# Kernel tuning notes

Hardware: AMD Instinct MI355X
Metric: run time of the kernel (lower is better)

The kernel has to match this reference:

```python
import jax, jax.numpy as jnp
import numpy as np

B, S, HID = 2, 2048, 2048
H, HKV, DH = 32, 8, 64
GROUPS = H // HKV
SCALE = DH ** -0.5
ROPE_THETA = 10000.0
NEG_INF = jnp.finfo(jnp.float32).min


def setup_inputs() -> dict:
    key = jax.random.key(0)
    ks = jax.random.split(key, 6)
    hidden_states = jax.random.normal(ks[0], (B, S, HID), dtype=jnp.float32)
    # true rotary embeddings (HF Llama style): inv_freq over half dim, duplicated
    inv_freq = 1.0 / (ROPE_THETA ** (np.arange(0, DH, 2, dtype=np.float32) / DH))
    freqs = np.arange(S, dtype=np.float32)[:, None] * inv_freq[None, :]  # [S, DH/2]
    emb = np.concatenate([freqs, freqs], axis=-1)                        # [S, DH]
    cos = jnp.broadcast_to(jnp.asarray(np.cos(emb), jnp.float32), (B, S, DH))
    sin = jnp.broadcast_to(jnp.asarray(np.sin(emb), jnp.float32), (B, S, DH))
    # additive causal mask [1,1,S,S]
    causal = jnp.tril(jnp.ones((S, S), dtype=bool))
    attention_mask = jnp.where(causal, 0.0, NEG_INF)[None, None].astype(jnp.float32)
    std = 0.02
    Wq = jax.random.normal(ks[1], (H * DH, HID), dtype=jnp.float32) * std
    Wk = jax.random.normal(ks[2], (HKV * DH, HID), dtype=jnp.float32) * std
    Wv = jax.random.normal(ks[3], (HKV * DH, HID), dtype=jnp.float32) * std
    Wo = jax.random.normal(ks[4], (HID, H * DH), dtype=jnp.float32) * std
    return {"hidden_states": hidden_states, "cos": cos, "sin": sin,
            "attention_mask": attention_mask, "Wq": Wq, "Wk": Wk, "Wv": Wv, "Wo": Wo}


def _rotate_half(x):
    x1, x2 = jnp.split(x, 2, axis=-1)
    return jnp.concatenate([-x2, x1], axis=-1)


def reference(hidden_states, cos, sin, attention_mask, Wq, Wk, Wv, Wo):
    b, s, _ = hidden_states.shape
    # projections -> [B, H(kv), S, DH]
    q = (hidden_states @ Wq.T).reshape(b, s, H, DH).transpose(0, 2, 1, 3)
    k = (hidden_states @ Wk.T).reshape(b, s, HKV, DH).transpose(0, 2, 1, 3)
    v = (hidden_states @ Wv.T).reshape(b, s, HKV, DH).transpose(0, 2, 1, 3)
    # RoPE (cos/sin: [B,S,DH] -> broadcast over head axis)
    c = cos[:, None, :, :]
    sn = sin[:, None, :, :]
    q = q * c + _rotate_half(q) * sn
    k = k * c + _rotate_half(k) * sn
    # GQA: repeat kv heads
    k = jnp.repeat(k, GROUPS, axis=1)  # [B,H,S,DH]
    v = jnp.repeat(v, GROUPS, axis=1)
    # eager attention: full [B,H,S,S] scores in memory
    scores = jnp.einsum('bhqd,bhkd->bhqk', q, k) * SCALE + attention_mask[:, :, :, :s]
    attn = jax.nn.softmax(scores, axis=-1)
    out = jnp.einsum('bhqk,bhkd->bhqd', attn, v)
    out = out.transpose(0, 2, 1, 3).reshape(b, s, H * DH)
    return out @ Wo.T
```

## Files before the change

### kernel.cpp

```cpp
#include <hip/hip_runtime.h>
#include <hip/hip_bf16.h>
#include <cstdint>
#include <cstddef>

#define B_    2
#define S_    2048
#define HID_  2048
#define H_    32
#define HKV_  8
#define DH_   64
#define SC2_  0.1803368801111244f

typedef __bf16 bf16;
typedef bf16  bf16x2 __attribute__((ext_vector_type(2)));
typedef bf16  bf16x4 __attribute__((ext_vector_type(4)));
typedef bf16  bf16x8 __attribute__((ext_vector_type(8)));
typedef float f32x4  __attribute__((ext_vector_type(4)));
typedef float f32x16 __attribute__((ext_vector_type(16)));
typedef uint32_t u32x2 __attribute__((ext_vector_type(2)));

typedef __attribute__((address_space(3))) uint32_t  lds_u32_t;
typedef __attribute__((address_space(1))) const uint32_t glob_u32_t;

__device__ __forceinline__ void async16(const void* g, void* l) {
    __builtin_amdgcn_global_load_lds((glob_u32_t*)g, (lds_u32_t*)l, 16, 0, 0);
}

__device__ __forceinline__ bf16x8 cvt8(float4 a, float4 b) {
    bf16x8 r;
    r[0] = (bf16)a.x; r[1] = (bf16)a.y; r[2] = (bf16)a.z; r[3] = (bf16)a.w;
    r[4] = (bf16)b.x; r[5] = (bf16)b.y; r[6] = (bf16)b.z; r[7] = (bf16)b.w;
    return r;
}

__device__ __forceinline__ uint32_t pkbf(float a, float b) {
    bf16x2 t; t[0] = (bf16)a; t[1] = (bf16)b;
    return __builtin_bit_cast(uint32_t, t);
}
__device__ __forceinline__ bf16x8 mk8(uint32_t a, uint32_t b, uint32_t c, uint32_t d) {
    union { uint32_t u[4]; bf16x8 v; } t;
    t.u[0] = a; t.u[1] = b; t.u[2] = c; t.u[3] = d;
    return t.v;
}

__global__ __launch_bounds__(256) void cvt_all_kernel(
    const float* __restrict__ X,  const float* __restrict__ Wq,
    const float* __restrict__ Wk, const float* __restrict__ Wv,
    const float* __restrict__ Wo,
    bf16* __restrict__ Xb,  bf16* __restrict__ Wqb, bf16* __restrict__ Wkb,
    bf16* __restrict__ Wvb, bf16* __restrict__ Wob)
{
    const int i = blockIdx.x * 256 + threadIdx.x;
    const float* src; bf16* dst; int off;
    if (i < 1048576)      { src = X;  dst = Xb;  off = i; }
    else if (i < 1572864) { src = Wq; dst = Wqb; off = i - 1048576; }
    else if (i < 1703936) { src = Wk; dst = Wkb; off = i - 1572864; }
    else if (i < 1835008) { src = Wv; dst = Wvb; off = i - 1703936; }
    else                  { src = Wo; dst = Wob; off = i - 1835008; }
    float4 a = ((const float4*)src)[2 * off];
    float4 b = ((const float4*)src)[2 * off + 1];
    ((bf16x8*)dst)[off] = cvt8(a, b);
}

__global__ __launch_bounds__(256) void gemm_qkv_kernel(
    const bf16* __restrict__ A,
    const bf16* __restrict__ Wqb, const bf16* __restrict__ Wkb,
    const bf16* __restrict__ Wvb,
    const float* __restrict__ cs, const float* __restrict__ sn,
    bf16* __restrict__ Qo, bf16* __restrict__ Ko, bf16* __restrict__ Vt)
{
    __shared__ bf16 a_lds[128 * 64];
    __shared__ bf16 b_lds[128 * 64];

    const int tid  = threadIdx.x;
    const int wave = tid >> 6;
    const int lane = tid & 63;
    const int quad = lane >> 4;
    const int l16  = lane & 15;
    const int wm   = wave >> 1;
    const int wn   = wave & 1;
    const int m0   = blockIdx.x * 128;
    const int n0   = blockIdx.y * 128;

    f32x4 acc[4][4];
    #pragma unroll
    for (int mt = 0; mt < 4; ++mt)
        #pragma unroll
        for (int nt = 0; nt < 4; ++nt)
            acc[mt][nt] = (f32x4){0.f, 0.f, 0.f, 0.f};

    int srow[4], sgcol[4];
    const bf16* browp[4];
    #pragma unroll
    for (int i = 0; i < 4; ++i) {
        const int e = tid * 8 + i * 2048;
        srow[i] = e >> 6;
        const int chunk = (e >> 3) & 7;
        sgcol[i] = (chunk ^ (srow[i] & 7)) << 3;
        const int n = n0 + srow[i];
        browp[i] = (n < 2048) ? (Wqb + (size_t)n * HID_)
                 : (n < 2560) ? (Wkb + (size_t)(n - 2048) * HID_)
                              : (Wvb + (size_t)(n - 2560) * HID_);
    }

    for (int k0 = 0; k0 < HID_; k0 += 64) {
        #pragma unroll
        for (int i = 0; i < 4; ++i) {
            async16(A + (size_t)(m0 + srow[i]) * HID_ + k0 + sgcol[i],
                    &a_lds[tid * 8 + i * 2048]);
            async16(browp[i] + k0 + sgcol[i],
                    &b_lds[tid * 8 + i * 2048]);
        }
        __syncthreads();
        #pragma unroll
        for (int ks = 0; ks < 2; ++ks) {
            bf16x8 af[4], bfr[4];
            #pragma unroll
            for (int mt = 0; mt < 4; ++mt) {
                const int row = wm * 64 + mt * 16 + l16;
                const int c = (ks * 4 + quad) ^ (row & 7);
                af[mt] = *(const bf16x8*)(&a_lds[row * 64 + c * 8]);
            }
            #pragma unroll
            for (int nt = 0; nt < 4; ++nt) {
                const int row = wn * 64 + nt * 16 + l16;
                const int c = (ks * 4 + quad) ^ (row & 7);
                bfr[nt] = *(const bf16x8*)(&b_lds[row * 64 + c * 8]);
            }
            #pragma unroll
            for (int mt = 0; mt < 4; ++mt)
                #pragma unroll
                for (int nt = 0; nt < 4; ++nt)
                    acc[mt][nt] = __builtin_amdgcn_mfma_f32_16x16x32_bf16(
                        af[mt], bfr[nt], acc[mt][nt], 0, 0, 0);
        }
        __syncthreads();
    }

    const int nw = n0 + wn * 64;
    const int d  = l16;
    #pragma unroll
    for (int mt = 0; mt < 4; ++mt) {
        #pragma unroll
        for (int r = 0; r < 4; ++r) {
            const int m  = m0 + wm * 64 + mt * 16 + quad * 4 + r;
            const int bb = m >> 11;
            const int ss = m & (S_ - 1);
            const float v0 = acc[mt][0][r], v1 = acc[mt][1][r];
            const float v2 = acc[mt][2][r], v3 = acc[mt][3][r];
            if (nw < 2048) {
                const int h = nw >> 6;
                bf16* dp = Qo + ((size_t)(bb * H_ + h) * S_ + ss) * DH_;
                const float* cp = cs + ((size_t)bb * S_ + ss) * DH_;
                const float* sp = sn + ((size_t)bb * S_ + ss) * DH_;
                dp[ 0 + d] = (bf16)((v0 * cp[ 0 + d] - v2 * sp[ 0 + d]) * SC2_);
                dp[16 + d] = (bf16)((v1 * cp[16 + d] - v3 * sp[16 + d]) * SC2_);
                dp[32 + d] = (bf16)((v2 * cp[32 + d] + v0 * sp[32 + d]) * SC2_);
                dp[48 + d] = (bf16)((v3 * cp[48 + d] + v1 * sp[48 + d]) * SC2_);
            } else if (nw < 2560) {
                const int h = (nw - 2048) >> 6;
                bf16* dp = Ko + ((size_t)(bb * HKV_ + h) * S_ + ss) * DH_;
                const float* cp = cs + ((size_t)bb * S_ + ss) * DH_;
                const float* sp = sn + ((size_t)bb * S_ + ss) * DH_;
                dp[ 0 + d] = (bf16)(v0 * cp[ 0 + d] - v2 * sp[ 0 + d]);
                dp[16 + d] = (bf16)(v1 * cp[16 + d] - v3 * sp[16 + d]);
                dp[32 + d] = (bf16)(v2 * cp[32 + d] + v0 * sp[32 + d]);
                dp[48 + d] = (bf16)(v3 * cp[48 + d] + v1 * sp[48 + d]);
            } else {
                const int h = (nw - 2560) >> 6;
                bf16* dp = Vt + ((size_t)(bb * HKV_ + h) * DH_) * S_ + ss;
                dp[(size_t)( 0 + d) * S_] = (bf16)v0;
                dp[(size_t)(16 + d) * S_] = (bf16)v1;
                dp[(size_t)(32 + d) * S_] = (bf16)v2;
                dp[(size_t)(48 + d) * S_] = (bf16)v3;
            }
        }
    }
}

__global__ __launch_bounds__(256) void gemm_out_kernel(
    const bf16* __restrict__ A, const bf16* __restrict__ Wb,
    float* __restrict__ Y)
{
    __shared__ bf16 a_lds[128 * 64];
    __shared__ bf16 b_lds[128 * 64];

    const int tid  = threadIdx.x;
    const int wave = tid >> 6;
    const int lane = tid & 63;
    const int quad = lane >> 4;
    const int l16  = lane & 15;
    const int wm   = wave >> 1;
    const int wn   = wave & 1;
    const int m0   = blockIdx.x * 128;
    const int n0   = blockIdx.y * 128;

    f32x4 acc[4][4];
    #pragma unroll
    for (int mt = 0; mt < 4; ++mt)
        #pragma unroll
        for (int nt = 0; nt < 4; ++nt)
            acc[mt][nt] = (f32x4){0.f, 0.f, 0.f, 0.f};

    int srow[4], sgcol[4];
    #pragma unroll
    for (int i = 0; i < 4; ++i) {
        const int e = tid * 8 + i * 2048;
        srow[i] = e >> 6;
        const int chunk = (e >> 3) & 7;
        sgcol[i] = (chunk ^ (srow[i] & 7)) << 3;
    }

    for (int k0 = 0; k0 < HID_; k0 += 64) {
        #pragma unroll
        for (int i = 0; i < 4; ++i) {
            async16(A + (size_t)(m0 + srow[i]) * HID_ + k0 + sgcol[i],
                    &a_lds[tid * 8 + i * 2048]);
            async16(Wb + (size_t)(n0 + srow[i]) * HID_ + k0 + sgcol[i],
                    &b_lds[tid * 8 + i * 2048]);
        }
        __syncthreads();
        #pragma unroll
        for (int ks = 0; ks < 2; ++ks) {
            bf16x8 af[4], bfr[4];
            #pragma unroll
            for (int mt = 0; mt < 4; ++mt) {
                const int row = wm * 64 + mt * 16 + l16;
                const int c = (ks * 4 + quad) ^ (row & 7);
                af[mt] = *(const bf16x8*)(&a_lds[row * 64 + c * 8]);
            }
            #pragma unroll
            for (int nt = 0; nt < 4; ++nt) {
                const int row = wn * 64 + nt * 16 + l16;
                const int c = (ks * 4 + quad) ^ (row & 7);
                bfr[nt] = *(const bf16x8*)(&b_lds[row * 64 + c * 8]);
            }
            #pragma unroll
            for (int mt = 0; mt < 4; ++mt)
                #pragma unroll
                for (int nt = 0; nt < 4; ++nt)
                    acc[mt][nt] = __builtin_amdgcn_mfma_f32_16x16x32_bf16(
                        af[mt], bfr[nt], acc[mt][nt], 0, 0, 0);
        }
        __syncthreads();
    }

    #pragma unroll
    for (int mt = 0; mt < 4; ++mt)
        #pragma unroll
        for (int nt = 0; nt < 4; ++nt)
            #pragma unroll
            for (int r = 0; r < 4; ++r) {
                const int m = m0 + wm * 64 + mt * 16 + quad * 4 + r;
                const int n = n0 + wn * 64 + nt * 16 + l16;
                Y[(size_t)m * HID_ + n] = acc[mt][nt][r];
            }
}

__global__ __launch_bounds__(256) void attn_kernel(
    const bf16* __restrict__ Q, const bf16* __restrict__ K,
    const bf16* __restrict__ Vt, bf16* __restrict__ O)
{
    __shared__ bf16 k_lds[2][64 * 64];
    __shared__ bf16 v_lds[2][64 * 64];

    const int tid  = threadIdx.x;
    const int wave = tid >> 6;
    const int lane = tid & 63;
    const int l32  = lane & 31;
    const int half = lane >> 5;
    const int h  = blockIdx.y;
    const int b  = blockIdx.z;
    const int hkv = h >> 2;

    const bf16* Qg = Q  + (size_t)(b * H_ + h) * S_ * DH_;
    const bf16* Kg = K  + (size_t)(b * HKV_ + hkv) * S_ * DH_;
    const bf16* Vg = Vt + ((size_t)(b * HKV_ + hkv) * DH_) * S_;

    const int srow0  = tid >> 3;
    const int scolsw = ((tid & 7) ^ ((tid >> 3) & 7)) << 3;

    #pragma unroll 1
    for (int ph = 0; ph < 2; ++ph) {
        const int qt  = ph == 0 ? (int)blockIdx.x : (15 - (int)blockIdx.x);
        const int q0  = qt * 128;
        const int qb0 = q0 + wave * 32;
        const int qa  = qb0 + l32;

        bf16x8 qf[4];
        #pragma unroll
        for (int c = 0; c < 4; ++c)
            qf[c] = *(const bf16x8*)(Qg + (size_t)qa * DH_ + c * 16 + half * 8);

        f32x16 o_acc[2];
        #pragma unroll
        for (int dt = 0; dt < 2; ++dt)
            #pragma unroll
            for (int e = 0; e < 16; ++e) o_acc[dt][e] = 0.f;
        float m_i = -1e30f, l_i = 0.f;

        const int nkt = 2 * qt + 2;

        #pragma unroll
        for (int i = 0; i < 2; ++i) {
            const int row = srow0 + i * 32;
            async16(Kg + (size_t)row * DH_ + scolsw, &k_lds[0][tid * 8 + i * 2048]);
            async16(Vg + (size_t)row * S_  + scolsw, &v_lds[0][tid * 8 + i * 2048]);
        }
        __syncthreads();

        for (int kt = 0; kt < nkt; ++kt) {
            if (kt + 1 < nkt) {
                bf16* kb = k_lds[(kt + 1) & 1];
                bf16* vb = v_lds[(kt + 1) & 1];
                #pragma unroll
                for (int i = 0; i < 2; ++i) {
                    const int row = srow0 + i * 32;
                    async16(Kg + (size_t)((kt + 1) * 64 + row) * DH_ + scolsw,
                            kb + tid * 8 + i * 2048);
                    async16(Vg + (size_t)row * S_ + (kt + 1) * 64 + scolsw,
                            vb + tid * 8 + i * 2048);
                }
            }

            if (kt * 64 <= qb0 + 31) {
                const bf16* kb = k_lds[kt & 1];
                const bf16* vb = v_lds[kt & 1];
                const bool act1 = (kt * 64 + 32) <= (qb0 + 31);

                f32x16 s0, s1;
                {
                    bf16x8 kf[4];
                    #pragma unroll
                    for (int c = 0; c < 4; ++c) {
                        const int col = ((2 * c + half) ^ (l32 & 7)) << 3;
                        kf[c] = *(const bf16x8*)(kb + l32 * 64 + col);
                    }
                    f32x16 a;
                    #pragma unroll
                    for (int e = 0; e < 16; ++e) a[e] = 0.f;
                    __builtin_amdgcn_s_setprio(1);
                    #pragma unroll
                    for (int c = 0; c < 4; ++c)
                        a = __builtin_amdgcn_mfma_f32_32x32x16_bf16(kf[c], qf[c], a, 0, 0, 0);
                    __builtin_amdgcn_s_setprio(0);
                    s0 = a;
                }
                if (act1) {
                    bf16x8 kf[4];
                    #pragma unroll
                    for (int c = 0; c < 4; ++c) {
                        const int row = 32 + l32;
                        const int col = ((2 * c + half) ^ (row & 7)) << 3;
                        kf[c] = *(const bf16x8*)(kb + row * 64 + col);
                    }
                    f32x16 a;
                    #pragma unroll
                    for (int e = 0; e < 16; ++e) a[e] = 0.f;
                    __builtin_amdgcn_s_setprio(1);
                    #pragma unroll
                    for (int c = 0; c < 4; ++c)
                        a = __builtin_amdgcn_mfma_f32_32x32x16_bf16(kf[c], qf[c], a, 0, 0, 0);
                    __builtin_amdgcn_s_setprio(0);
                    s1 = a;
                }

                if (!((kt * 64 + 31) <= qb0)) {
                    const int qrel = qa - kt * 64 - 4 * half;
                    #pragma unroll
                    for (int e = 0; e < 16; ++e)
                        if (((e & 3) + 8 * (e >> 2)) > qrel) s0[e] = -1e30f;
                }
                if (act1 && !((kt * 64 + 63) <= qb0)) {
                    const int qrel = qa - kt * 64 - 32 - 4 * half;
                    #pragma unroll
                    for (int e = 0; e < 16; ++e)
                        if (((e & 3) + 8 * (e >> 2)) > qrel) s1[e] = -1e30f;
                }

                float mx = s0[0];
                #pragma unroll
                for (int e = 1; e < 16; ++e) mx = fmaxf(mx, s0[e]);
                if (act1)
                    #pragma unroll
                    for (int e = 0; e < 16; ++e) mx = fmaxf(mx, s1[e]);
                mx = fmaxf(mx, __shfl_xor(mx, 32));

                float al = 1.f;
                if (!__all(mx <= m_i + 8.f)) {
                    const float mn = fmaxf(m_i, mx);
                    al = exp2f(m_i - mn);
                    m_i = mn;
                    #pragma unroll
                    for (int dt = 0; dt < 2; ++dt)
                        #pragma unroll
                        for (int e = 0; e < 16; ++e) o_acc[dt][e] *= al;
                }

                float sm = 0.f;
                #pragma unroll
                for (int e = 0; e < 16; ++e) {
                    const float pp = exp2f(s0[e] - m_i);
                    s0[e] = pp; sm += pp;
                }
                if (act1)
                    #pragma unroll
                    for (int e = 0; e < 16; ++e) {
                        const float pp = exp2f(s1[e] - m_i);
                        s1[e] = pp; sm += pp;
                    }
                sm += __shfl_xor(sm, 32);
                l_i = l_i * al + sm;

                bf16x8 pf[4];
                {
                    uint32_t d0 = pkbf(s0[0],  s0[1]),  d1 = pkbf(s0[2],  s0[3]);
                    uint32_t d2 = pkbf(s0[4],  s0[5]),  d3 = pkbf(s0[6],  s0[7]);
                    uint32_t d4 = pkbf(s0[8],  s0[9]),  d5 = pkbf(s0[10], s0[11]);
                    uint32_t d6 = pkbf(s0[12], s0[13]), d7 = pkbf(s0[14], s0[15]);
                    u32x2 r02 = __builtin_amdgcn_permlane32_swap(d0, d2, false, false);
                    u32x2 r13 = __builtin_amdgcn_permlane32_swap(d1, d3, false, false);
                    u32x2 r46 = __builtin_amdgcn_permlane32_swap(d4, d6, false, false);
                    u32x2 r57 = __builtin_amdgcn_permlane32_swap(d5, d7, false, false);
                    pf[0] = mk8(r02[0], r13[0], r02[1], r13[1]);
                    pf[1] = mk8(r46[0], r57[0], r46[1], r57[1]);
                }
                if (act1) {
                    uint32_t d0 = pkbf(s1[0],  s1[1]),  d1 = pkbf(s1[2],  s1[3]);
                    uint32_t d2 = pkbf(s1[4],  s1[5]),  d3 = pkbf(s1[6],  s1[7]);
                    uint32_t d4 = pkbf(s1[8],  s1[9]),  d5 = pkbf(s1[10], s1[11]);
                    uint32_t d6 = pkbf(s1[12], s1[13]), d7 = pkbf(s1[14], s1[15]);
                    u32x2 r02 = __builtin_amdgcn_permlane32_swap(d0, d2, false, false);
                    u32x2 r13 = __builtin_amdgcn_permlane32_swap(d1, d3, false, false);
                    u32x2 r46 = __builtin_amdgcn_permlane32_swap(d4, d6, false, false);
                    u32x2 r57 = __builtin_amdgcn_permlane32_swap(d5, d7, false, false);
                    pf[2] = mk8(r02[0], r13[0], r02[1], r13[1]);
                    pf[3] = mk8(r46[0], r57[0], r46[1], r57[1]);
                }

                bf16x8 vf[2][4];
                #pragma unroll
                for (int dt = 0; dt < 2; ++dt)
                    #pragma unroll
                    for (int c = 0; c < 4; ++c) {
                        const int row = dt * 32 + l32;
                        const int col = ((2 * c + half) ^ (row & 7)) << 3;
                        vf[dt][c] = *(const bf16x8*)(vb + row * 64 + col);
                    }

                const int nc = act1 ? 4 : 2;
                __builtin_amdgcn_s_setprio(1);
                #pragma unroll
                for (int c = 0; c < 4; ++c) {
                    if (c >= nc) break;
                    #pragma unroll
                    for (int dt = 0; dt < 2; ++dt)
                        o_acc[dt] = __builtin_amdgcn_mfma_f32_32x32x16_bf16(
                            vf[dt][c], pf[c], o_acc[dt], 0, 0, 0);
                }
                __builtin_amdgcn_s_setprio(0);
            }
            __syncthreads();
        }

        const float inv = 1.f / l_i;
        bf16* op = O + ((size_t)(b * S_ + qa) * H_ + h) * DH_;
        #pragma unroll
        for (int dt = 0; dt < 2; ++dt)
            #pragma unroll
            for (int g = 0; g < 4; ++g) {
                bf16x4 ov;
                #pragma unroll
                for (int r = 0; r < 4; ++r) ov[r] = (bf16)(o_acc[dt][g * 4 + r] * inv);
                *(bf16x4*)(op + dt * 32 + g * 8 + half * 4) = ov;
            }
        __syncthreads();
    }
}

extern "C" void kernel_launch(void* const* d_in, const int* in_sizes, int n_in,
                              void* d_out, int out_size, void* d_ws, size_t ws_size,
                              hipStream_t stream)
{
    const float* X    = (const float*)d_in[0];
    const float* cs   = (const float*)d_in[1];
    const float* sn   = (const float*)d_in[2];
    const float* Wq   = (const float*)d_in[4];
    const float* Wk   = (const float*)d_in[5];
    const float* Wv   = (const float*)d_in[6];
    const float* Wo   = (const float*)d_in[7];
    float* Y          = (float*)d_out;

    bf16* Xb  = (bf16*)d_ws;
    bf16* Wqb = Xb  + (size_t)8388608;
    bf16* Wkb = Wqb + (size_t)4194304;
    bf16* Wvb = Wkb + (size_t)1048576;
    bf16* Wob = Wvb + (size_t)1048576;
    bf16* Qb  = Wob + (size_t)4194304;
    bf16* Kb  = Qb  + (size_t)8388608;
    bf16* Vtb = Kb  + (size_t)2097152;
    bf16* Ob  = Vtb + (size_t)2097152;

    dim3 blk(256);
    cvt_all_kernel<<<dim3(9216), blk, 0, stream>>>(X, Wq, Wk, Wv, Wo,
                                                   Xb, Wqb, Wkb, Wvb, Wob);
    gemm_qkv_kernel<<<dim3(32, 24), blk, 0, stream>>>(Xb, Wqb, Wkb, Wvb,
                                                      cs, sn, Qb, Kb, Vtb);
    attn_kernel<<<dim3(8, H_, B_), blk, 0, stream>>>(Qb, Kb, Vtb, Ob);
    gemm_out_kernel<<<dim3(32, 16), blk, 0, stream>>>(Ob, Wob, Y);
}
```

Baseline: 354.1 us.

## Double-buffer LDS tiles and swizzle block order in projection GEMMs

Both the QKV and output projection GEMMs now keep two LDS buffers, prefetching the next K tile asynchronously while MFMA work runs on the current one. The aim is to hide global-to-LDS latency behind compute. Block indices are also remapped with an XCD-aware swizzle (idx&7 times the per-XCD count) so neighbouring tiles that share A/B rows land on the same XCD's L2. LDS use per block doubles, which may lower occupancy.

```diff
diff --git a/kernel.cpp b/kernel.cpp
--- a/kernel.cpp
+++ b/kernel.cpp
@@ -69,8 +69,8 @@
     const float* __restrict__ cs, const float* __restrict__ sn,
     bf16* __restrict__ Qo, bf16* __restrict__ Ko, bf16* __restrict__ Vt)
 {
-    __shared__ bf16 a_lds[128 * 64];
-    __shared__ bf16 b_lds[128 * 64];
+    __shared__ bf16 a_lds[2][128 * 64];
+    __shared__ bf16 b_lds[2][128 * 64];
 
     const int tid  = threadIdx.x;
     const int wave = tid >> 6;
@@ -79,8 +79,11 @@
     const int l16  = lane & 15;
     const int wm   = wave >> 1;
     const int wn   = wave & 1;
-    const int m0   = blockIdx.x * 128;
-    const int n0   = blockIdx.y * 128;
+
+    const int idx = blockIdx.x + 32 * blockIdx.y;
+    const int swz = (idx & 7) * 96 + (idx >> 3);
+    const int m0  = (swz & 31) * 128;
+    const int n0  = (swz >> 5) * 128;
 
     f32x4 acc[4][4];
     #pragma unroll
@@ -103,15 +106,28 @@
                               : (Wvb + (size_t)(n - 2560) * HID_);
     }
 
+    #pragma unroll
+    for (int i = 0; i < 4; ++i) {
+        async16(A + (size_t)(m0 + srow[i]) * HID_ + sgcol[i],
+                &a_lds[0][tid * 8 + i * 2048]);
+        async16(browp[i] + sgcol[i],
+                &b_lds[0][tid * 8 + i * 2048]);
+    }
+    __syncthreads();
+
     for (int k0 = 0; k0 < HID_; k0 += 64) {
-        #pragma unroll
-        for (int i = 0; i < 4; ++i) {
-            async16(A + (size_t)(m0 + srow[i]) * HID_ + k0 + sgcol[i],
-                    &a_lds[tid * 8 + i * 2048]);
-            async16(browp[i] + k0 + sgcol[i],
-                    &b_lds[tid * 8 + i * 2048]);
-        }
-        __syncthreads();
+        const int cur = (k0 >> 6) & 1;
+        if (k0 + 64 < HID_) {
+            #pragma unroll
+            for (int i = 0; i < 4; ++i) {
+                async16(A + (size_t)(m0 + srow[i]) * HID_ + k0 + 64 + sgcol[i],
+                        &a_lds[cur ^ 1][tid * 8 + i * 2048]);
+                async16(browp[i] + k0 + 64 + sgcol[i],
+                        &b_lds[cur ^ 1][tid * 8 + i * 2048]);
+            }
+        }
+        const bf16* al = a_lds[cur];
+        const bf16* bl = b_lds[cur];
         #pragma unroll
         for (int ks = 0; ks < 2; ++ks) {
             bf16x8 af[4], bfr[4];
@@ -119,13 +135,13 @@
             for (int mt = 0; mt < 4; ++mt) {
                 const int row = wm * 64 + mt * 16 + l16;
                 const int c = (ks * 4 + quad) ^ (row & 7);
-                af[mt] = *(const bf16x8*)(&a_lds[row * 64 + c * 8]);
+                af[mt] = *(const bf16x8*)(&al[row * 64 + c * 8]);
             }
             #pragma unroll
             for (int nt = 0; nt < 4; ++nt) {
                 const int row = wn * 64 + nt * 16 + l16;
                 const int c = (ks * 4 + quad) ^ (row & 7);
-                bfr[nt] = *(const bf16x8*)(&b_lds[row * 64 + c * 8]);
+                bfr[nt] = *(const bf16x8*)(&bl[row * 64 + c * 8]);
             }
             #pragma unroll
             for (int mt = 0; mt < 4; ++mt)
@@ -182,8 +198,8 @@
     const bf16* __restrict__ A, const bf16* __restrict__ Wb,
     float* __restrict__ Y)
 {
-    __shared__ bf16 a_lds[128 * 64];
-    __shared__ bf16 b_lds[128 * 64];
+    __shared__ bf16 a_lds[2][128 * 64];
+    __shared__ bf16 b_lds[2][128 * 64];
 
     const int tid  = threadIdx.x;
     const int wave = tid >> 6;
@@ -192,8 +208,11 @@
     const int l16  = lane & 15;
     const int wm   = wave >> 1;
     const int wn   = wave & 1;
-    const int m0   = blockIdx.x * 128;
-    const int n0   = blockIdx.y * 128;
+
+    const int idx = blockIdx.x + 32 * blockIdx.y;
+    const int swz = (idx & 7) * 64 + (idx >> 3);
+    const int m0  = (swz & 31) * 128;
+    const int n0  = (swz >> 5) * 128;
 
     f32x4 acc[4][4];
     #pragma unroll
@@ -211,15 +230,28 @@
         sgcol[i] = (chunk ^ (srow[i] & 7)) << 3;
     }
 
+    #pragma unroll
+    for (int i = 0; i < 4; ++i) {
+        async16(A + (size_t)(m0 + srow[i]) * HID_ + sgcol[i],
+                &a_lds[0][tid * 8 + i * 2048]);
+        async16(Wb + (size_t)(n0 + srow[i]) * HID_ + sgcol[i],
+                &b_lds[0][tid * 8 + i * 2048]);
+    }
+    __syncthreads();
+
     for (int k0 = 0; k0 < HID_; k0 += 64) {
-        #pragma unroll
-        for (int i = 0; i < 4; ++i) {
-            async16(A + (size_t)(m0 + srow[i]) * HID_ + k0 + sgcol[i],
-                    &a_lds[tid * 8 + i * 2048]);
-            async16(Wb + (size_t)(n0 + srow[i]) * HID_ + k0 + sgcol[i],
-                    &b_lds[tid * 8 + i * 2048]);
-        }
-        __syncthreads();
+        const int cur = (k0 >> 6) & 1;
+        if (k0 + 64 < HID_) {
+            #pragma unroll
+            for (int i = 0; i < 4; ++i) {
+                async16(A + (size_t)(m0 + srow[i]) * HID_ + k0 + 64 + sgcol[i],
+                        &a_lds[cur ^ 1][tid * 8 + i * 2048]);
+                async16(Wb + (size_t)(n0 + srow[i]) * HID_ + k0 + 64 + sgcol[i],
+                        &b_lds[cur ^ 1][tid * 8 + i * 2048]);
+            }
+        }
+        const bf16* al = a_lds[cur];
+        const bf16* bl = b_lds[cur];
         #pragma unroll
         for (int ks = 0; ks < 2; ++ks) {
             bf16x8 af[4], bfr[4];
@@ -227,13 +259,13 @@
             for (int mt = 0; mt < 4; ++mt) {
                 const int row = wm * 64 + mt * 16 + l16;
                 const int c = (ks * 4 + quad) ^ (row & 7);
-                af[mt] = *(const bf16x8*)(&a_lds[row * 64 + c * 8]);
+                af[mt] = *(const bf16x8*)(&al[row * 64 + c * 8]);
             }
             #pragma unroll
             for (int nt = 0; nt < 4; ++nt) {
                 const int row = wn * 64 + nt * 16 + l16;
                 const int c = (ks * 4 + quad) ^ (row & 7);
-                bfr[nt] = *(const bf16x8*)(&b_lds[row * 64 + c * 8]);
+                bfr[nt] = *(const bf16x8*)(&bl[row * 64 + c * 8]);
             }
             #pragma unroll
             for (int mt = 0; mt < 4; ++mt)
```

Result: no change. 349.0 us (-1.4%).
